# Optimization experiments

Hardware: AMD Instinct MI355X
Metric: run time of the kernel (lower is better)

Reference implementation:

```python
import jax, jax.numpy as jnp
import numpy as np

B, S, D, H = 4, 2048, 1024, 16
DH = D // H


def setup_inputs() -> dict:
    key = jax.random.key(0)
    k1, k2, k3, k4, k5 = jax.random.split(key, 5)
    scale = 1.0 / np.sqrt(D)
    return {
        "x": jax.random.normal(k1, (B, S, D), dtype=jnp.float32),
        "w_in": jax.random.normal(k2, (3 * D, D), dtype=jnp.float32) * scale,
        "b_in": jax.random.normal(k3, (3 * D,), dtype=jnp.float32) * 0.01,
        "w_out": jax.random.normal(k4, (D, D), dtype=jnp.float32) * scale,
        "b_out": jax.random.normal(k5, (D,), dtype=jnp.float32) * 0.01,
        "causal_mask": 1,
    }


def reference(x, w_in, b_in, w_out, b_out, causal_mask):
    batch, seq, d = x.shape
    # fused QKV projection: [B,S,3D]
    qkv = jnp.einsum('bsd,ed->bse', x, w_in) + b_in
    q, k, v = jnp.split(qkv, 3, axis=-1)
    # [B,S,H,DH]
    q = q.reshape(batch, seq, H, DH)
    k = k.reshape(batch, seq, H, DH)
    v = v.reshape(batch, seq, H, DH)
    # scaled dot-product attention, scale = 1/sqrt(d_head)
    scores = jnp.einsum('bqhd,bkhd->bhqk', q, k) / jnp.sqrt(jnp.asarray(DH, dtype=x.dtype))
    if causal_mask:  # static Python bool/int, matches is_causal semantics
        mask = jnp.tril(jnp.ones((seq, seq), dtype=bool))
        scores = jnp.where(mask, scores, jnp.asarray(-jnp.inf, dtype=scores.dtype))
    attn = jax.nn.softmax(scores, axis=-1)
    out = jnp.einsum('bhqk,bkhd->bqhd', attn, v).reshape(batch, seq, d)
    return jnp.einsum('bsd,ed->bse', out, w_out) + b_out
```

## Files before the change

kernel.cpp:

```cpp
#include <hip/hip_runtime.h>
#include <hip/hip_bf16.h>
#include <stdint.h>

constexpr int kB  = 4;
constexpr int kS  = 2048;
constexpr int kD  = 1024;
constexpr int kH  = 16;
constexpr int kDH = 64;
constexpr int kM  = kB * kS;
constexpr int k3D = 3 * kD;

constexpr float kQscale = 0.18033688011112042f;

typedef __attribute__((ext_vector_type(8))) short short8;
typedef __attribute__((ext_vector_type(4))) float f32x4;

__device__ __forceinline__ float exp2v(float x) {
  return __builtin_amdgcn_exp2f(x);
}

__device__ __forceinline__ unsigned short f2bf(float f) {
  unsigned u = __float_as_uint(f);
  u += 0x7fffu + ((u >> 16) & 1u);
  return (unsigned short)(u >> 16);
}

__device__ __forceinline__ unsigned cvtpk2bf(float lo, float hi) {
  unsigned r;
  asm("v_cvt_pk_bf16_f32 %0, %1, %2" : "=v"(r) : "v"(lo), "v"(hi));
  return r;
}

__device__ __forceinline__ void async16(const void* g, void* l) {
  __builtin_amdgcn_global_load_lds(
      (const __attribute__((address_space(1))) unsigned int*)g,
      (__attribute__((address_space(3))) unsigned int*)l, 16, 0, 0);
}

__global__ __launch_bounds__(256) void cvt_bf16_3(
    const float* __restrict__ x, const float* __restrict__ wi,
    const float* __restrict__ wo, unsigned short* __restrict__ xb,
    unsigned short* __restrict__ wib, unsigned short* __restrict__ wob) {
  constexpr int n_x  = kM * kD / 4;
  constexpr int n_wi = k3D * kD / 4;
  int i = blockIdx.x * 256 + threadIdx.x;
  const float* src;
  unsigned short* dst;
  int j;
  if (i < n_x)            { src = x;  dst = xb;  j = i; }
  else if (i < n_x + n_wi){ src = wi; dst = wib; j = i - n_x; }
  else                    { src = wo; dst = wob; j = i - n_x - n_wi; }
  float4 v = ((const float4*)src)[j];
  ushort4 r;
  r.x = f2bf(v.x); r.y = f2bf(v.y); r.z = f2bf(v.z); r.w = f2bf(v.w);
  ((ushort4*)dst)[j] = r;
}

template <bool OUT_BF16, bool QSCALE, bool VT>
__global__ __launch_bounds__(512, 2) void gemm_mfma_256(
    const unsigned short* __restrict__ A, int lda,
    const unsigned short* __restrict__ Bt, int ldb,
    const float* __restrict__ bias, void* __restrict__ Cp, int ldc, int K,
    unsigned short* __restrict__ vtbp) {
  __shared__ unsigned short SL[65536];
  auto Asl = (unsigned short(*)[16384])(SL);
  auto Bsl = (unsigned short(*)[16384])(SL + 32768);
  const int t = threadIdx.x;
  const int lane = t & 63, l15 = lane & 15, quad = lane >> 4, w = t >> 6;

  const int nwg = gridDim.x * gridDim.y;
  int bid = blockIdx.y * gridDim.x + blockIdx.x;
  if ((nwg & 7) == 0) bid = (bid & 7) * (nwg >> 3) + (bid >> 3);
  const int bx = bid % gridDim.x, by = bid / gridDim.x;
  const int row0 = by * 256, col0 = bx * 256;
  const int wm = (w & 1) * 128, wn = (w >> 1) * 64;

  f32x4 acc[8][4] = {};

  const unsigned short* gA[2][2];
  const unsigned short* gB[2][2];
#pragma unroll
  for (int h = 0; h < 2; ++h)
#pragma unroll
    for (int ss = 0; ss < 2; ++ss) {
      const int s = t + ss * 512;
      const int r = s >> 3, c = (s & 7) ^ (r & 7);
      gA[h][ss] = A  + (size_t)(row0 + h * 128 + r) * lda + c * 8;
      gB[h][ss] = Bt + (size_t)(col0 + h * 128 + r) * ldb + c * 8;
    }

#define STG_A(h, buf, k0)                                              \
  do {                                                                 \
    async16(gA[h][0] + (k0), Asl[buf] + (h) * 8192 + t * 8);           \
    async16(gA[h][1] + (k0), Asl[buf] + (h) * 8192 + (t + 512) * 8);   \
  } while (0)
#define STG_B(h, buf, k0)                                              \
  do {                                                                 \
    async16(gB[h][0] + (k0), Bsl[buf] + (h) * 8192 + t * 8);           \
    async16(gB[h][1] + (k0), Bsl[buf] + (h) * 8192 + (t + 512) * 8);   \
  } while (0)

#define ARD(mq, mt, ks)                                                  \
  (*(const short8*)(as + (wm + (mq) * 64 + (mt) * 16 + l15) * 64 +       \
                    ((((ks) * 4 + quad) ^ (l15 & 7)) * 8)))
#define BRD(nq, nt, ks)                                                  \
  (*(const short8*)(bs + (wn + (nq) * 32 + (nt) * 16 + l15) * 64 +       \
                    ((((ks) * 4 + quad) ^ (l15 & 7)) * 8)))

  const int nkt = K / 64;
  STG_A(0, 0, 0); STG_A(1, 0, 0); STG_B(0, 0, 0); STG_B(1, 0, 0);

  short8 af[2][4][2];
  short8 bf[2][2];

  for (int kt = 0; kt < nkt; ++kt) {
    const int buf = kt & 1, nbuf = buf ^ 1;
    const int k0n = (kt + 1) * 64;
    const bool pf = (kt + 1 < nkt);
    const unsigned short* as = Asl[buf];
    const unsigned short* bs = Bsl[buf];

    asm volatile("s_waitcnt vmcnt(0)" ::: "memory");
    __builtin_amdgcn_s_barrier();
    __builtin_amdgcn_sched_barrier(0);

    if (pf) STG_A(0, nbuf, k0n);
#pragma unroll
    for (int mt = 0; mt < 4; ++mt)
#pragma unroll
      for (int ks = 0; ks < 2; ++ks) af[0][mt][ks] = ARD(0, mt, ks);
#pragma unroll
    for (int nt = 0; nt < 2; ++nt)
#pragma unroll
      for (int ks = 0; ks < 2; ++ks) bf[nt][ks] = BRD(0, nt, ks);
    __builtin_amdgcn_s_setprio(1);
#pragma unroll
    for (int mt = 0; mt < 4; ++mt)
#pragma unroll
      for (int nt = 0; nt < 2; ++nt)
#pragma unroll
        for (int ks = 0; ks < 2; ++ks)
          acc[mt][nt] = __builtin_amdgcn_mfma_f32_16x16x32_bf16(
              af[0][mt][ks], bf[nt][ks], acc[mt][nt], 0, 0, 0);
    __builtin_amdgcn_s_setprio(0);

    if (pf) STG_A(1, nbuf, k0n);
#pragma unroll
    for (int mt = 0; mt < 4; ++mt)
#pragma unroll
      for (int ks = 0; ks < 2; ++ks) af[1][mt][ks] = ARD(1, mt, ks);
    __builtin_amdgcn_s_setprio(1);
#pragma unroll
    for (int mt = 0; mt < 4; ++mt)
#pragma unroll
      for (int nt = 0; nt < 2; ++nt)
#pragma unroll
        for (int ks = 0; ks < 2; ++ks)
          acc[4 + mt][nt] = __builtin_amdgcn_mfma_f32_16x16x32_bf16(
              af[1][mt][ks], bf[nt][ks], acc[4 + mt][nt], 0, 0, 0);
    __builtin_amdgcn_s_setprio(0);

    if (pf) STG_B(0, nbuf, k0n);
#pragma unroll
    for (int nt = 0; nt < 2; ++nt)
#pragma unroll
      for (int ks = 0; ks < 2; ++ks) bf[nt][ks] = BRD(1, nt, ks);
    __builtin_amdgcn_s_setprio(1);
#pragma unroll
    for (int mt = 0; mt < 4; ++mt)
#pragma unroll
      for (int nt = 0; nt < 2; ++nt)
#pragma unroll
        for (int ks = 0; ks < 2; ++ks)
          acc[4 + mt][2 + nt] = __builtin_amdgcn_mfma_f32_16x16x32_bf16(
              af[1][mt][ks], bf[nt][ks], acc[4 + mt][2 + nt], 0, 0, 0);
    __builtin_amdgcn_s_setprio(0);

    if (pf) STG_B(1, nbuf, k0n);
    __builtin_amdgcn_s_setprio(1);
#pragma unroll
    for (int mt = 0; mt < 4; ++mt)
#pragma unroll
      for (int nt = 0; nt < 2; ++nt)
#pragma unroll
        for (int ks = 0; ks < 2; ++ks)
          acc[mt][2 + nt] = __builtin_amdgcn_mfma_f32_16x16x32_bf16(
              af[0][mt][ks], bf[nt][ks], acc[mt][2 + nt], 0, 0, 0);
    __builtin_amdgcn_s_setprio(0);
  }
#undef STG_A
#undef STG_B
#undef ARD
#undef BRD

  float bv[4];
#pragma unroll
  for (int n = 0; n < 4; ++n)
    bv[n] = bias[col0 + wn + (n >> 1) * 32 + (n & 1) * 16 + l15];

  if (VT && col0 >= 2 * kD) {
    __syncthreads();
#pragma unroll
    for (int m = 0; m < 8; ++m)
#pragma unroll
      for (int n = 0; n < 4; ++n) {
        const int cl = wn + (n >> 1) * 32 + (n & 1) * 16 + l15;
        const int u = (wm >> 2) + (m >> 2) * 16 + (m & 3) * 4 + quad;
        uint2 pk = make_uint2(
            cvtpk2bf(acc[m][n][0] + bv[n], acc[m][n][1] + bv[n]),
            cvtpk2bf(acc[m][n][2] + bv[n], acc[m][n][3] + bv[n]));
        *(uint2*)(SL + cl * 256 + ((u ^ (cl & 15)) << 2)) = pk;
      }
    __syncthreads();
    const int b_ = by >> 3, s0 = (by & 7) * 256;
    const int lhalf = lane >> 5, l31 = lane & 31;
#pragma unroll
    for (int ps = 0; ps < 16; ++ps) {
      const int cl = ps * 16 + w * 2 + lhalf;
      uint2 v0 = *(const uint2*)(SL + cl * 256 +
                                 (((l31 * 2) ^ (cl & 15)) << 2));
      uint2 v1 = *(const uint2*)(SL + cl * 256 +
                                 (((l31 * 2 + 1) ^ (cl & 15)) << 2));
      uint4 vv = make_uint4(v0.x, v0.y, v1.x, v1.y);
      unsigned short* gd =
          vtbp + (size_t)(b_ * 1024 + col0 - 2 * kD + cl) * kS + s0 + l31 * 8;
      *(uint4*)gd = vv;
    }
    return;
  }

  const float sc = (QSCALE && col0 < kD) ? kQscale : 1.0f;
#pragma unroll
  for (int m = 0; m < 8; ++m)
#pragma unroll
    for (int i = 0; i < 4; ++i) {
      const size_t r =
          (size_t)(row0 + wm + (m >> 2) * 64 + (m & 3) * 16 + quad * 4 + i);
#pragma unroll
      for (int n = 0; n < 4; ++n) {
        float v = (acc[m][n][i] + bv[n]) * sc;
        const size_t cidx =
            r * (size_t)ldc + col0 + wn + (n >> 1) * 32 + (n & 1) * 16 + l15;
        if (OUT_BF16) ((unsigned short*)Cp)[cidx] = f2bf(v);
        else          ((float*)Cp)[cidx] = v;
      }
    }
}

template <bool OUT_BF16, bool QSCALE>
__global__ __launch_bounds__(256) void gemm_mfma_128(
    const unsigned short* __restrict__ A, int lda,
    const unsigned short* __restrict__ Bt, int ldb,
    const float* __restrict__ bias, void* __restrict__ Cp, int ldc, int K) {
  __shared__ unsigned short As[2][4096];
  __shared__ unsigned short Bs[2][4096];
  const int t = threadIdx.x;
  const int lane = t & 63, l15 = lane & 15, quad = lane >> 4, w = t >> 6;

  const int nwg = gridDim.x * gridDim.y;
  int bid = blockIdx.y * gridDim.x + blockIdx.x;
  if ((nwg & 7) == 0) bid = (bid & 7) * (nwg >> 3) + (bid >> 3);
  const int bx = bid % gridDim.x, by = bid / gridDim.x;

  const int row0 = by * 128, col0 = bx * 128;
  const int wm = (w & 1) * 64, wn = (w >> 1) * 64;

  f32x4 acc[4][4] = {};

  const int q1 = t, q2 = t + 256;
  const unsigned short* a1 = A  + (size_t)(row0 + (q1 & 127)) * lda + (q1 >> 7) * 8;
  const unsigned short* a2 = A  + (size_t)(row0 + (q2 & 127)) * lda + (q2 >> 7) * 8;
  const unsigned short* b1 = Bt + (size_t)(col0 + (q1 & 127)) * ldb + (q1 >> 7) * 8;
  const unsigned short* b2 = Bt + (size_t)(col0 + (q2 & 127)) * ldb + (q2 >> 7) * 8;

  const int nIter = K / 32;
  async16(a1, As[0] + q1 * 8);
  async16(a2, As[0] + q2 * 8);
  async16(b1, Bs[0] + q1 * 8);
  async16(b2, Bs[0] + q2 * 8);

  for (int it = 0; it < nIter; ++it) {
    __syncthreads();
    const int cb = it & 1, nb = cb ^ 1;
    if (it + 1 < nIter) {
      const int k0 = (it + 1) * 32;
      async16(a1 + k0, As[nb] + q1 * 8);
      async16(a2 + k0, As[nb] + q2 * 8);
      async16(b1 + k0, Bs[nb] + q1 * 8);
      async16(b2 + k0, Bs[nb] + q2 * 8);
    }
    short8 af[4], bf[4];
#pragma unroll
    for (int mt = 0; mt < 4; ++mt)
      af[mt] = *(const short8*)(As[cb] + (quad * 128 + wm + mt * 16 + l15) * 8);
#pragma unroll
    for (int nt = 0; nt < 4; ++nt)
      bf[nt] = *(const short8*)(Bs[cb] + (quad * 128 + wn + nt * 16 + l15) * 8);
#pragma unroll
    for (int mt = 0; mt < 4; ++mt)
#pragma unroll
      for (int nt = 0; nt < 4; ++nt)
        acc[mt][nt] = __builtin_amdgcn_mfma_f32_16x16x32_bf16(
            af[mt], bf[nt], acc[mt][nt], 0, 0, 0);
  }

  const float sc = (QSCALE && col0 < kD) ? kQscale : 1.0f;
  float bv[4];
#pragma unroll
  for (int nt = 0; nt < 4; ++nt) bv[nt] = bias[col0 + wn + nt * 16 + l15];
#pragma unroll
  for (int mt = 0; mt < 4; ++mt)
#pragma unroll
    for (int i = 0; i < 4; ++i) {
      const size_t r = (size_t)(row0 + wm + mt * 16 + quad * 4 + i);
#pragma unroll
      for (int nt = 0; nt < 4; ++nt) {
        float v = (acc[mt][nt][i] + bv[nt]) * sc;
        const size_t cidx = r * (size_t)ldc + col0 + wn + nt * 16 + l15;
        if (OUT_BF16) ((unsigned short*)Cp)[cidx] = f2bf(v);
        else          ((float*)Cp)[cidx] = v;
      }
    }
}

__global__ __launch_bounds__(256, 4) void flash_attn_mfma(
    unsigned short* __restrict__ qkvb, const unsigned short* __restrict__ vtb,
    const int* __restrict__ cflag) {
  __shared__ unsigned short QP[4096];
  __shared__ unsigned short Ks[2][4096];
  __shared__ unsigned short Vt[2][4096];

  const int lin = blockIdx.x;
  const int pr = lin >> 6;
  const int g  = ((lin >> 3) & 7) * 8 + (lin & 7);
  const int h = g & 15, b = g >> 4;
  const int t = threadIdx.x;
  const int lane = t & 63, l15 = lane & 15, quad = lane >> 4, w = t >> 6;
  const bool causal = (*cflag) != 0;

  unsigned short* qbase = qkvb + (size_t)(b * kS) * k3D + h * kDH;
  const unsigned short* vbase = vtb + (size_t)((b * kH + h) * kDH) * kS;
  const int c0 = t, c1 = t + 256;

  for (int half = 0; half < 2; ++half) {
    const int qt = half ? (31 - pr) : pr;
    const int q0 = qt * 64;
    const int ntiles = causal ? (qt + 1) : 32;

    async16(qbase + (size_t)(q0 + (c0 & 63)) * k3D + (c0 >> 6) * 8, QP + c0 * 8);
    async16(qbase + (size_t)(q0 + (c1 & 63)) * k3D + (c1 >> 6) * 8, QP + c1 * 8);
    async16(qbase + kD + (size_t)(c0 & 63) * k3D + (c0 >> 6) * 8, Ks[0] + c0 * 8);
    async16(qbase + kD + (size_t)(c1 & 63) * k3D + (c1 >> 6) * 8, Ks[0] + c1 * 8);
    async16(vbase + (size_t)(c0 & 63) * kS + (c0 >> 6) * 8, Vt[0] + c0 * 8);
    async16(vbase + (size_t)(c1 & 63) * kS + (c1 >> 6) * 8, Vt[0] + c1 * 8);
    __syncthreads();

    short8 bq[2];
#pragma unroll
    for (int kf = 0; kf < 2; ++kf)
      bq[kf] = *(const short8*)(
          QP + ((kf * 4 + quad) * 64 + w * 16 + l15) * 8);

    f32x4 O[4] = {};
    float m_i = -3.0e38f, l_i = 0.f;

    for (int kt = 0; kt < ntiles; ++kt) {
      const int cb = kt & 1, nb = cb ^ 1;
      const int kk0 = kt * 64;

      if (kt + 1 < ntiles) {
        const int kn = kk0 + 64;
        async16(qbase + kD + (size_t)(kn + (c0 & 63)) * k3D + (c0 >> 6) * 8,
                Ks[nb] + c0 * 8);
        async16(qbase + kD + (size_t)(kn + (c1 & 63)) * k3D + (c1 >> 6) * 8,
                Ks[nb] + c1 * 8);
        async16(vbase + (size_t)(c0 & 63) * kS + kn + (c0 >> 6) * 8,
                Vt[nb] + c0 * 8);
        async16(vbase + (size_t)(c1 & 63) * kS + kn + (c1 >> 6) * 8,
                Vt[nb] + c1 * 8);
      }

      f32x4 s[4];
      __builtin_amdgcn_s_setprio(1);
#pragma unroll
      for (int mt = 0; mt < 4; ++mt) {
        short8 a0 = *(const short8*)(Ks[cb] + ((quad)*64 + mt * 16 + l15) * 8);
        short8 a1 =
            *(const short8*)(Ks[cb] + ((4 + quad) * 64 + mt * 16 + l15) * 8);
        f32x4 z = {};
        z = __builtin_amdgcn_mfma_f32_16x16x32_bf16(a0, bq[0], z, 0, 0, 0);
        z = __builtin_amdgcn_mfma_f32_16x16x32_bf16(a1, bq[1], z, 0, 0, 0);
        s[mt] = z;
      }
      __builtin_amdgcn_s_setprio(0);

      const int gq = q0 + w * 16 + l15;
      if (causal && kt == ntiles - 1) {
#pragma unroll
        for (int mt = 0; mt < 4; ++mt)
#pragma unroll
          for (int i = 0; i < 4; ++i)
            if (kk0 + mt * 16 + quad * 4 + i > gq) s[mt][i] = -3.0e38f;
      }
      float mx = -3.0e38f;
#pragma unroll
      for (int mt = 0; mt < 4; ++mt)
#pragma unroll
        for (int i = 0; i < 4; ++i) mx = fmaxf(mx, s[mt][i]);
      mx = fmaxf(mx, __shfl_xor(mx, 16));
      mx = fmaxf(mx, __shfl_xor(mx, 32));

      if (!__all(mx <= m_i + 8.0f)) {
        const float mn = fmaxf(m_i, mx);
        const float alpha = exp2v(m_i - mn);
        m_i = mn;
        l_i *= alpha;
#pragma unroll
        for (int i = 0; i < 4; ++i) {
          const float a = __shfl(alpha, quad * 4 + i);
#pragma unroll
          for (int ntd = 0; ntd < 4; ++ntd) O[ntd][i] *= a;
        }
      }

      float p[4][4];
      float rs = 0.f;
#pragma unroll
      for (int mt = 0; mt < 4; ++mt)
#pragma unroll
        for (int i = 0; i < 4; ++i) {
          p[mt][i] = exp2v(s[mt][i] - m_i);
          rs += p[mt][i];
        }
      rs += __shfl_xor(rs, 16);
      rs += __shfl_xor(rs, 32);
      l_i += rs;

#pragma unroll
      for (int mt = 0; mt < 4; ++mt) {
        uint2 pk = make_uint2(cvtpk2bf(p[mt][0], p[mt][1]),
                              cvtpk2bf(p[mt][2], p[mt][3]));
        *(uint2*)(QP + ((mt * 2 + (quad >> 1)) * 64 + w * 16 + l15) * 8 +
                  (quad & 1) * 4) = pk;
      }

      __builtin_amdgcn_s_setprio(1);
#pragma unroll
      for (int kf = 0; kf < 2; ++kf) {
        short8 aP = *(const short8*)(
            QP + ((kf * 4 + quad) * 64 + w * 16 + l15) * 8);
#pragma unroll
        for (int ntd = 0; ntd < 4; ++ntd) {
          short8 bV = *(const short8*)(
              Vt[cb] + ((kf * 4 + quad) * 64 + ntd * 16 + l15) * 8);
          O[ntd] = __builtin_amdgcn_mfma_f32_16x16x32_bf16(
              aP, bV, O[ntd], 0, 0, 0);
        }
      }
      __builtin_amdgcn_s_setprio(0);

      __syncthreads();
    }

#pragma unroll
    for (int i = 0; i < 4; ++i) {
      const float linv = 1.0f / __shfl(l_i, quad * 4 + i);
      unsigned short* dst =
          qbase + (size_t)(q0 + w * 16 + quad * 4 + i) * k3D;
#pragma unroll
      for (int ntd = 0; ntd < 4; ++ntd)
        dst[ntd * 16 + l15] = f2bf(O[ntd][i] * linv);
    }
  }
}

extern "C" void kernel_launch(void* const* d_in, const int* in_sizes, int n_in,
                              void* d_out, int out_size, void* d_ws,
                              size_t ws_size, hipStream_t stream) {
  const float* x     = (const float*)d_in[0];
  const float* w_in  = (const float*)d_in[1];
  const float* b_in  = (const float*)d_in[2];
  const float* w_out = (const float*)d_in[3];
  const float* b_out = (const float*)d_in[4];
  const int*   cfl   = (const int*)d_in[5];
  float* out = (float*)d_out;

  char* ws = (char*)d_ws;
  unsigned short* qkvb = (unsigned short*)(ws);
  unsigned short* xb   = (unsigned short*)(ws + 50331648);
  unsigned short* wib  = (unsigned short*)(ws + 67108864);
  unsigned short* wob  = (unsigned short*)(ws + 73400320);
  unsigned short* vtb  = (unsigned short*)(ws + 75497472);

  cvt_bf16_3<<<(kM * kD + k3D * kD + kD * kD) / 4 / 256, 256, 0, stream>>>(
      x, w_in, w_out, xb, wib, wob);

  gemm_mfma_256<true, true, true><<<dim3(k3D / 256, kM / 256), 512, 0, stream>>>(
      xb, kD, wib, kD, b_in, qkvb, k3D, kD, vtb);

  flash_attn_mfma<<<dim3(16 * kH * kB), 256, 0, stream>>>(qkvb, vtb, cfl);

  gemm_mfma_128<false, false><<<dim3(kD / 128, kM / 128), 256, 0, stream>>>(
      qkvb, k3D, wob, kD, b_out, out, kD, kD);
}
```

Before: 271.2 us.

## Halve GEMM K-tile to 32 to cut LDS and raise occupancy

The 256x256 bf16 GEMM now stages K=32 slices instead of K=64, halving the shared-memory footprint to 64 KB, and the launch bound asks for 4 waves-per-EU occupancy instead of 2. The V-transpose epilogue is split into two 128-column passes so it fits in the smaller LDS buffer. The aim is more resident workgroups to hide latency, at the cost of twice as many barriers and k-iterations, less MFMA work per sync, and a tighter register budget that may cause spills with 128 accumulator floats per thread.

```diff
diff --git a/kernel.cpp b/kernel.cpp
--- a/kernel.cpp
+++ b/kernel.cpp
@@ -57,14 +57,14 @@
 }
 
 template <bool OUT_BF16, bool QSCALE, bool VT>
-__global__ __launch_bounds__(512, 2) void gemm_mfma_256(
+__global__ __launch_bounds__(512, 4) void gemm_mfma_256(
     const unsigned short* __restrict__ A, int lda,
     const unsigned short* __restrict__ Bt, int ldb,
     const float* __restrict__ bias, void* __restrict__ Cp, int ldc, int K,
     unsigned short* __restrict__ vtbp) {
-  __shared__ unsigned short SL[65536];
-  auto Asl = (unsigned short(*)[16384])(SL);
-  auto Bsl = (unsigned short(*)[16384])(SL + 32768);
+  __shared__ unsigned short SL[32768];
+  auto Asl = (unsigned short(*)[8192])(SL);
+  auto Bsl = (unsigned short(*)[8192])(SL + 16384);
   const int t = threadIdx.x;
   const int lane = t & 63, l15 = lane & 15, quad = lane >> 4, w = t >> 6;
 
@@ -77,45 +77,40 @@
 
   f32x4 acc[8][4] = {};
 
-  const unsigned short* gA[2][2];
-  const unsigned short* gB[2][2];
-#pragma unroll
-  for (int h = 0; h < 2; ++h)
-#pragma unroll
-    for (int ss = 0; ss < 2; ++ss) {
-      const int s = t + ss * 512;
-      const int r = s >> 3, c = (s & 7) ^ (r & 7);
-      gA[h][ss] = A  + (size_t)(row0 + h * 128 + r) * lda + c * 8;
-      gB[h][ss] = Bt + (size_t)(col0 + h * 128 + r) * ldb + c * 8;
-    }
-
-#define STG_A(h, buf, k0)                                              \
-  do {                                                                 \
-    async16(gA[h][0] + (k0), Asl[buf] + (h) * 8192 + t * 8);           \
-    async16(gA[h][1] + (k0), Asl[buf] + (h) * 8192 + (t + 512) * 8);   \
+  const unsigned short* gA[2];
+  const unsigned short* gB[2];
+#pragma unroll
+  for (int ss = 0; ss < 2; ++ss) {
+    const int s = t + ss * 512;
+    const int r = s >> 2, c = (s & 3) ^ (r & 3);
+    gA[ss] = A  + (size_t)(row0 + r) * lda + c * 8;
+    gB[ss] = Bt + (size_t)(col0 + r) * ldb + c * 8;
+  }
+
+#define STG_ALL(buf, k0)                                       \
+  do {                                                         \
+    async16(gA[0] + (k0), Asl[buf] + t * 8);                   \
+    async16(gA[1] + (k0), Asl[buf] + (t + 512) * 8);           \
+    async16(gB[0] + (k0), Bsl[buf] + t * 8);                   \
+    async16(gB[1] + (k0), Bsl[buf] + (t + 512) * 8);           \
   } while (0)
-#define STG_B(h, buf, k0)                                              \
-  do {                                                                 \
-    async16(gB[h][0] + (k0), Bsl[buf] + (h) * 8192 + t * 8);           \
-    async16(gB[h][1] + (k0), Bsl[buf] + (h) * 8192 + (t + 512) * 8);   \
-  } while (0)
-
-#define ARD(mq, mt, ks)                                                  \
-  (*(const short8*)(as + (wm + (mq) * 64 + (mt) * 16 + l15) * 64 +       \
-                    ((((ks) * 4 + quad) ^ (l15 & 7)) * 8)))
-#define BRD(nq, nt, ks)                                                  \
-  (*(const short8*)(bs + (wn + (nq) * 32 + (nt) * 16 + l15) * 64 +       \
-                    ((((ks) * 4 + quad) ^ (l15 & 7)) * 8)))
-
-  const int nkt = K / 64;
-  STG_A(0, 0, 0); STG_A(1, 0, 0); STG_B(0, 0, 0); STG_B(1, 0, 0);
-
-  short8 af[2][4][2];
+
+#define ARD(mq, mt)                                                      \
+  (*(const short8*)(as + (wm + (mq) * 64 + (mt) * 16 + l15) * 32 +       \
+                    (((quad) ^ (l15 & 3)) * 8)))
+#define BRD(nq, nt)                                                      \
+  (*(const short8*)(bs + (wn + (nq) * 32 + (nt) * 16 + l15) * 32 +       \
+                    (((quad) ^ (l15 & 3)) * 8)))
+
+  const int nkt = K / 32;
+  STG_ALL(0, 0);
+
+  short8 af[2][4];
   short8 bf[2][2];
 
   for (int kt = 0; kt < nkt; ++kt) {
     const int buf = kt & 1, nbuf = buf ^ 1;
-    const int k0n = (kt + 1) * 64;
+    const int k0n = (kt + 1) * 32;
     const bool pf = (kt + 1 < nkt);
     const unsigned short* as = Asl[buf];
     const unsigned short* bs = Bsl[buf];
@@ -124,72 +119,53 @@
     __builtin_amdgcn_s_barrier();
     __builtin_amdgcn_sched_barrier(0);
 
-    if (pf) STG_A(0, nbuf, k0n);
-#pragma unroll
-    for (int mt = 0; mt < 4; ++mt)
-#pragma unroll
-      for (int ks = 0; ks < 2; ++ks) af[0][mt][ks] = ARD(0, mt, ks);
-#pragma unroll
-    for (int nt = 0; nt < 2; ++nt)
-#pragma unroll
-      for (int ks = 0; ks < 2; ++ks) bf[nt][ks] = BRD(0, nt, ks);
+    if (pf) STG_ALL(nbuf, k0n);
+
+#pragma unroll
+    for (int mt = 0; mt < 4; ++mt) af[0][mt] = ARD(0, mt);
+#pragma unroll
+    for (int nt = 0; nt < 2; ++nt) bf[0][nt] = BRD(0, nt);
     __builtin_amdgcn_s_setprio(1);
 #pragma unroll
     for (int mt = 0; mt < 4; ++mt)
 #pragma unroll
       for (int nt = 0; nt < 2; ++nt)
-#pragma unroll
-        for (int ks = 0; ks < 2; ++ks)
-          acc[mt][nt] = __builtin_amdgcn_mfma_f32_16x16x32_bf16(
-              af[0][mt][ks], bf[nt][ks], acc[mt][nt], 0, 0, 0);
+        acc[mt][nt] = __builtin_amdgcn_mfma_f32_16x16x32_bf16(
+            af[0][mt], bf[0][nt], acc[mt][nt], 0, 0, 0);
     __builtin_amdgcn_s_setprio(0);
 
-    if (pf) STG_A(1, nbuf, k0n);
-#pragma unroll
-    for (int mt = 0; mt < 4; ++mt)
-#pragma unroll
-      for (int ks = 0; ks < 2; ++ks) af[1][mt][ks] = ARD(1, mt, ks);
+#pragma unroll
+    for (int mt = 0; mt < 4; ++mt) af[1][mt] = ARD(1, mt);
     __builtin_amdgcn_s_setprio(1);
 #pragma unroll
     for (int mt = 0; mt < 4; ++mt)
 #pragma unroll
       for (int nt = 0; nt < 2; ++nt)
-#pragma unroll
-        for (int ks = 0; ks < 2; ++ks)
-          acc[4 + mt][nt] = __builtin_amdgcn_mfma_f32_16x16x32_bf16(
-              af[1][mt][ks], bf[nt][ks], acc[4 + mt][nt], 0, 0, 0);
+        acc[4 + mt][nt] = __builtin_amdgcn_mfma_f32_16x16x32_bf16(
+            af[1][mt], bf[0][nt], acc[4 + mt][nt], 0, 0, 0);
     __builtin_amdgcn_s_setprio(0);
 
-    if (pf) STG_B(0, nbuf, k0n);
-#pragma unroll
-    for (int nt = 0; nt < 2; ++nt)
-#pragma unroll
-      for (int ks = 0; ks < 2; ++ks) bf[nt][ks] = BRD(1, nt, ks);
+#pragma unroll
+    for (int nt = 0; nt < 2; ++nt) bf[1][nt] = BRD(1, nt);
     __builtin_amdgcn_s_setprio(1);
 #pragma unroll
     for (int mt = 0; mt < 4; ++mt)
 #pragma unroll
       for (int nt = 0; nt < 2; ++nt)
-#pragma unroll
-        for (int ks = 0; ks < 2; ++ks)
-          acc[4 + mt][2 + nt] = __builtin_amdgcn_mfma_f32_16x16x32_bf16(
-              af[1][mt][ks], bf[nt][ks], acc[4 + mt][2 + nt], 0, 0, 0);
+        acc[4 + mt][2 + nt] = __builtin_amdgcn_mfma_f32_16x16x32_bf16(
+            af[1][mt], bf[1][nt], acc[4 + mt][2 + nt], 0, 0, 0);
     __builtin_amdgcn_s_setprio(0);
 
-    if (pf) STG_B(1, nbuf, k0n);
     __builtin_amdgcn_s_setprio(1);
 #pragma unroll
     for (int mt = 0; mt < 4; ++mt)
 #pragma unroll
       for (int nt = 0; nt < 2; ++nt)
-#pragma unroll
-        for (int ks = 0; ks < 2; ++ks)
-          acc[mt][2 + nt] = __builtin_amdgcn_mfma_f32_16x16x32_bf16(
-              af[0][mt][ks], bf[nt][ks], acc[mt][2 + nt], 0, 0, 0);
+        acc[mt][2 + nt] = __builtin_amdgcn_mfma_f32_16x16x32_bf16(
+            af[0][mt], bf[1][nt], acc[mt][2 + nt], 0, 0, 0);
     __builtin_amdgcn_s_setprio(0);
   }
-#undef STG_A
-#undef STG_B
+#undef STG_ALL
 #undef ARD
 #undef BRD
 
@@ -199,32 +175,39 @@
     bv[n] = bias[col0 + wn + (n >> 1) * 32 + (n & 1) * 16 + l15];
 
   if (VT && col0 >= 2 * kD) {
-    __syncthreads();
-#pragma unroll
-    for (int m = 0; m < 8; ++m)
-#pragma unroll
-      for (int n = 0; n < 4; ++n) {
-        const int cl = wn + (n >> 1) * 32 + (n & 1) * 16 + l15;
-        const int u = (wm >> 2) + (m >> 2) * 16 + (m & 3) * 4 + quad;
-        uint2 pk = make_uint2(
-            cvtpk2bf(acc[m][n][0] + bv[n], acc[m][n][1] + bv[n]),
-            cvtpk2bf(acc[m][n][2] + bv[n], acc[m][n][3] + bv[n]));
-        *(uint2*)(SL + cl * 256 + ((u ^ (cl & 15)) << 2)) = pk;
-      }
-    __syncthreads();
     const int b_ = by >> 3, s0 = (by & 7) * 256;
     const int lhalf = lane >> 5, l31 = lane & 31;
 #pragma unroll
-    for (int ps = 0; ps < 16; ++ps) {
-      const int cl = ps * 16 + w * 2 + lhalf;
-      uint2 v0 = *(const uint2*)(SL + cl * 256 +
-                                 (((l31 * 2) ^ (cl & 15)) << 2));
-      uint2 v1 = *(const uint2*)(SL + cl * 256 +
-                                 (((l31 * 2 + 1) ^ (cl & 15)) << 2));
-      uint4 vv = make_uint4(v0.x, v0.y, v1.x, v1.y);
-      unsigned short* gd =
-          vtbp + (size_t)(b_ * 1024 + col0 - 2 * kD + cl) * kS + s0 + l31 * 8;
-      *(uint4*)gd = vv;
+    for (int p = 0; p < 2; ++p) {
+      __syncthreads();
+      if ((w >> 2) == p) {
+#pragma unroll
+        for (int m = 0; m < 8; ++m)
+#pragma unroll
+          for (int n = 0; n < 4; ++n) {
+            const int clp =
+                (wn - p * 128) + (n >> 1) * 32 + (n & 1) * 16 + l15;
+            const int u = (wm >> 2) + (m >> 2) * 16 + (m & 3) * 4 + quad;
+            uint2 pk = make_uint2(
+                cvtpk2bf(acc[m][n][0] + bv[n], acc[m][n][1] + bv[n]),
+                cvtpk2bf(acc[m][n][2] + bv[n], acc[m][n][3] + bv[n]));
+            *(uint2*)(SL + clp * 256 + ((u ^ (clp & 15)) << 2)) = pk;
+          }
+      }
+      __syncthreads();
+#pragma unroll
+      for (int ps = 0; ps < 8; ++ps) {
+        const int clp = ps * 16 + w * 2 + lhalf;
+        uint2 v0 = *(const uint2*)(SL + clp * 256 +
+                                   (((l31 * 2) ^ (clp & 15)) << 2));
+        uint2 v1 = *(const uint2*)(SL + clp * 256 +
+                                   (((l31 * 2 + 1) ^ (clp & 15)) << 2));
+        uint4 vv = make_uint4(v0.x, v0.y, v1.x, v1.y);
+        unsigned short* gd =
+            vtbp + (size_t)(b_ * 1024 + col0 - 2 * kD + p * 128 + clp) * kS +
+            s0 + l31 * 8;
+        *(uint4*)gd = vv;
+      }
     }
     return;
   }
```

New measurement: 723.4 us. 2.67x slower.

## Enlarge flash-attention query tile to 128 rows with 8 waves sharing K/V

Applied to the files above, without the earlier changes.

Doubles the attention block to 512 threads covering 128 query rows, so each K/V tile loaded into shared memory is reused by twice as many waves, halving K/V global traffic per query. Each wave skips score/PV work for causally fully-masked key tiles and applies masking on any diagonal-straddling tile. Grid shrinks to half the blocks, which may reduce load balance and adds idle waves near the diagonal.

```diff
diff --git a/kernel.cpp b/kernel.cpp
--- a/kernel.cpp
+++ b/kernel.cpp
@@ -323,10 +323,10 @@
     }
 }
 
-__global__ __launch_bounds__(256, 4) void flash_attn_mfma(
+__global__ __launch_bounds__(512, 4) void flash_attn_mfma(
     unsigned short* __restrict__ qkvb, const unsigned short* __restrict__ vtb,
     const int* __restrict__ cflag) {
-  __shared__ unsigned short QP[4096];
+  __shared__ unsigned short QP[8192];
   __shared__ unsigned short Ks[2][4096];
   __shared__ unsigned short Vt[2][4096];
 
@@ -340,29 +340,29 @@
 
   unsigned short* qbase = qkvb + (size_t)(b * kS) * k3D + h * kDH;
   const unsigned short* vbase = vtb + (size_t)((b * kH + h) * kDH) * kS;
-  const int c0 = t, c1 = t + 256;
 
   for (int half = 0; half < 2; ++half) {
-    const int qt = half ? (31 - pr) : pr;
-    const int q0 = qt * 64;
-    const int ntiles = causal ? (qt + 1) : 32;
-
-    async16(qbase + (size_t)(q0 + (c0 & 63)) * k3D + (c0 >> 6) * 8, QP + c0 * 8);
-    async16(qbase + (size_t)(q0 + (c1 & 63)) * k3D + (c1 >> 6) * 8, QP + c1 * 8);
-    async16(qbase + kD + (size_t)(c0 & 63) * k3D + (c0 >> 6) * 8, Ks[0] + c0 * 8);
-    async16(qbase + kD + (size_t)(c1 & 63) * k3D + (c1 >> 6) * 8, Ks[0] + c1 * 8);
-    async16(vbase + (size_t)(c0 & 63) * kS + (c0 >> 6) * 8, Vt[0] + c0 * 8);
-    async16(vbase + (size_t)(c1 & 63) * kS + (c1 >> 6) * 8, Vt[0] + c1 * 8);
+    const int qt = half ? (15 - pr) : pr;
+    const int q0 = qt * 128;
+    const int ntiles = causal ? (2 * qt + 2) : 32;
+
+    async16(qbase + (size_t)(q0 + (t & 127)) * k3D + (t >> 7) * 8, QP + t * 8);
+    async16(qbase + (size_t)(q0 + ((t + 512) & 127)) * k3D +
+                ((t + 512) >> 7) * 8,
+            QP + (t + 512) * 8);
+    async16(qbase + kD + (size_t)(t & 63) * k3D + (t >> 6) * 8, Ks[0] + t * 8);
+    async16(vbase + (size_t)(t & 63) * kS + (t >> 6) * 8, Vt[0] + t * 8);
     __syncthreads();
 
     short8 bq[2];
 #pragma unroll
     for (int kf = 0; kf < 2; ++kf)
       bq[kf] = *(const short8*)(
-          QP + ((kf * 4 + quad) * 64 + w * 16 + l15) * 8);
+          QP + ((kf * 4 + quad) * 128 + w * 16 + l15) * 8);
 
     f32x4 O[4] = {};
     float m_i = -3.0e38f, l_i = 0.f;
+    const int gqw = q0 + w * 16;
 
     for (int kt = 0; kt < ntiles; ++kt) {
       const int cb = kt & 1, nb = cb ^ 1;
@@ -370,94 +370,94 @@
 
       if (kt + 1 < ntiles) {
         const int kn = kk0 + 64;
-        async16(qbase + kD + (size_t)(kn + (c0 & 63)) * k3D + (c0 >> 6) * 8,
-                Ks[nb] + c0 * 8);
-        async16(qbase + kD + (size_t)(kn + (c1 & 63)) * k3D + (c1 >> 6) * 8,
-                Ks[nb] + c1 * 8);
-        async16(vbase + (size_t)(c0 & 63) * kS + kn + (c0 >> 6) * 8,
-                Vt[nb] + c0 * 8);
-        async16(vbase + (size_t)(c1 & 63) * kS + kn + (c1 >> 6) * 8,
-                Vt[nb] + c1 * 8);
+        async16(qbase + kD + (size_t)(kn + (t & 63)) * k3D + (t >> 6) * 8,
+                Ks[nb] + t * 8);
+        async16(vbase + (size_t)(t & 63) * kS + kn + (t >> 6) * 8,
+                Vt[nb] + t * 8);
       }
 
-      f32x4 s[4];
-      __builtin_amdgcn_s_setprio(1);
-#pragma unroll
-      for (int mt = 0; mt < 4; ++mt) {
-        short8 a0 = *(const short8*)(Ks[cb] + ((quad)*64 + mt * 16 + l15) * 8);
-        short8 a1 =
-            *(const short8*)(Ks[cb] + ((4 + quad) * 64 + mt * 16 + l15) * 8);
-        f32x4 z = {};
-        z = __builtin_amdgcn_mfma_f32_16x16x32_bf16(a0, bq[0], z, 0, 0, 0);
-        z = __builtin_amdgcn_mfma_f32_16x16x32_bf16(a1, bq[1], z, 0, 0, 0);
-        s[mt] = z;
+      const bool act = !causal || (kk0 <= gqw + 15);
+      if (act) {
+        f32x4 s[4];
+        __builtin_amdgcn_s_setprio(1);
+#pragma unroll
+        for (int mt = 0; mt < 4; ++mt) {
+          short8 a0 =
+              *(const short8*)(Ks[cb] + ((quad)*64 + mt * 16 + l15) * 8);
+          short8 a1 =
+              *(const short8*)(Ks[cb] + ((4 + quad) * 64 + mt * 16 + l15) * 8);
+          f32x4 z = {};
+          z = __builtin_amdgcn_mfma_f32_16x16x32_bf16(a0, bq[0], z, 0, 0, 0);
+          z = __builtin_amdgcn_mfma_f32_16x16x32_bf16(a1, bq[1], z, 0, 0, 0);
+          s[mt] = z;
+        }
+        __builtin_amdgcn_s_setprio(0);
+
+        const int gq = gqw + l15;
+        if (causal && kk0 + 63 > gqw) {
+#pragma unroll
+          for (int mt = 0; mt < 4; ++mt)
+#pragma unroll
+            for (int i = 0; i < 4; ++i)
+              if (kk0 + mt * 16 + quad * 4 + i > gq) s[mt][i] = -3.0e38f;
+        }
+        float mx = -3.0e38f;
+#pragma unroll
+        for (int mt = 0; mt < 4; ++mt)
+#pragma unroll
+          for (int i = 0; i < 4; ++i) mx = fmaxf(mx, s[mt][i]);
+        mx = fmaxf(mx, __shfl_xor(mx, 16));
+        mx = fmaxf(mx, __shfl_xor(mx, 32));
+
+        if (!__all(mx <= m_i + 8.0f)) {
+          const float mn = fmaxf(m_i, mx);
+          const float alpha = exp2v(m_i - mn);
+          m_i = mn;
+          l_i *= alpha;
+#pragma unroll
+          for (int i = 0; i < 4; ++i) {
+            const float a = __shfl(alpha, quad * 4 + i);
+#pragma unroll
+            for (int ntd = 0; ntd < 4; ++ntd) O[ntd][i] *= a;
+          }
+        }
+
+        float p[4][4];
+        float rs = 0.f;
+#pragma unroll
+        for (int mt = 0; mt < 4; ++mt)
+#pragma unroll
+          for (int i = 0; i < 4; ++i) {
+            p[mt][i] = exp2v(s[mt][i] - m_i);
+            rs += p[mt][i];
+          }
+        rs += __shfl_xor(rs, 16);
+        rs += __shfl_xor(rs, 32);
+        l_i += rs;
+
+#pragma unroll
+        for (int mt = 0; mt < 4; ++mt) {
+          uint2 pk = make_uint2(cvtpk2bf(p[mt][0], p[mt][1]),
+                                cvtpk2bf(p[mt][2], p[mt][3]));
+          *(uint2*)(QP + ((mt * 2 + (quad >> 1)) * 128 + w * 16 + l15) * 8 +
+                    (quad & 1) * 4) = pk;
+        }
+
+        __builtin_amdgcn_s_setprio(1);
+#pragma unroll
+        for (int kf = 0; kf < 2; ++kf) {
+          short8 aP = *(const short8*)(
+              QP + ((kf * 4 + quad) * 128 + w * 16 + l15) * 8);
+#pragma unroll
+          for (int ntd = 0; ntd < 4; ++ntd) {
+            short8 bV = *(const short8*)(
+                Vt[cb] + ((kf * 4 + quad) * 64 + ntd * 16 + l15) * 8);
+            O[ntd] = __builtin_amdgcn_mfma_f32_16x16x32_bf16(
+                aP, bV, O[ntd], 0, 0, 0);
+          }
+        }
+        __builtin_amdgcn_s_setprio(0);
       }
-      __builtin_amdgcn_s_setprio(0);
-
-      const int gq = q0 + w * 16 + l15;
-      if (causal && kt == ntiles - 1) {
-#pragma unroll
-        for (int mt = 0; mt < 4; ++mt)
-#pragma unroll
-          for (int i = 0; i < 4; ++i)
-            if (kk0 + mt * 16 + quad * 4 + i > gq) s[mt][i] = -3.0e38f;
-      }
-      float mx = -3.0e38f;
-#pragma unroll
-      for (int mt = 0; mt < 4; ++mt)
-#pragma unroll
-        for (int i = 0; i < 4; ++i) mx = fmaxf(mx, s[mt][i]);
-      mx = fmaxf(mx, __shfl_xor(mx, 16));
-      mx = fmaxf(mx, __shfl_xor(mx, 32));
-
-      if (!__all(mx <= m_i + 8.0f)) {
-        const float mn = fmaxf(m_i, mx);
-        const float alpha = exp2v(m_i - mn);
-        m_i = mn;
-        l_i *= alpha;
-#pragma unroll
-        for (int i = 0; i < 4; ++i) {
-          const float a = __shfl(alpha, quad * 4 + i);
-#pragma unroll
-          for (int ntd = 0; ntd < 4; ++ntd) O[ntd][i] *= a;
-        }
-      }
-
-      float p[4][4];
-      float rs = 0.f;
-#pragma unroll
-      for (int mt = 0; mt < 4; ++mt)
-#pragma unroll
-        for (int i = 0; i < 4; ++i) {
-          p[mt][i] = exp2v(s[mt][i] - m_i);
-          rs += p[mt][i];
-        }
-      rs += __shfl_xor(rs, 16);
-      rs += __shfl_xor(rs, 32);
-      l_i += rs;
-
-#pragma unroll
-      for (int mt = 0; mt < 4; ++mt) {
-        uint2 pk = make_uint2(cvtpk2bf(p[mt][0], p[mt][1]),
-                              cvtpk2bf(p[mt][2], p[mt][3]));
-        *(uint2*)(QP + ((mt * 2 + (quad >> 1)) * 64 + w * 16 + l15) * 8 +
-                  (quad & 1) * 4) = pk;
-      }
-
-      __builtin_amdgcn_s_setprio(1);
-#pragma unroll
-      for (int kf = 0; kf < 2; ++kf) {
-        short8 aP = *(const short8*)(
-            QP + ((kf * 4 + quad) * 64 + w * 16 + l15) * 8);
-#pragma unroll
-        for (int ntd = 0; ntd < 4; ++ntd) {
-          short8 bV = *(const short8*)(
-              Vt[cb] + ((kf * 4 + quad) * 64 + ntd * 16 + l15) * 8);
-          O[ntd] = __builtin_amdgcn_mfma_f32_16x16x32_bf16(
-              aP, bV, O[ntd], 0, 0, 0);
-        }
-      }
-      __builtin_amdgcn_s_setprio(0);
 
       __syncthreads();
     }
@@ -498,7 +498,7 @@
   gemm_mfma_256<true, true, true><<<dim3(k3D / 256, kM / 256), 512, 0, stream>>>(
       xb, kD, wib, kD, b_in, qkvb, k3D, kD, vtb);
 
-  flash_attn_mfma<<<dim3(16 * kH * kB), 256, 0, stream>>>(qkvb, vtb, cfl);
+  flash_attn_mfma<<<dim3(8 * kH * kB), 512, 0, stream>>>(qkvb, vtb, cfl);
 
   gemm_mfma_128<false, false><<<dim3(kD / 128, kM / 128), 256, 0, stream>>>(
       qkvb, k3D, wob, kD, b_out, out, kD, kD);
```

New measurement: 256.2 us. 1.06x faster.
